# Optimization experiments

Measured on AMD Instinct MI355X. Metric: run time of the kernel, lower is better.

The kernel has to match this reference:

```python
import jax, jax.numpy as jnp
import numpy as np
import math

B, T, C, TF, N, DK = 4, 2048, 768, 128, 8, 96  # DK = max(C//8,16)

def _tau_init(Tw):
    alpha = 0.1 ** (1.0 / max(Tw - 1, 1))
    tau = -math.log(max(alpha, 1e-10))
    return math.log(math.exp(tau) - 1 + 1e-10)

def setup_inputs() -> dict:
    key = jax.random.key(0)
    ks = jax.random.split(key, 13)
    w = lambda k, shp: jax.random.normal(k, shp, jnp.float32) * 0.02
    return {
        'x': jax.random.normal(ks[0], (B, T, C), jnp.float32),
        'tau_gate': jnp.float32(_tau_init(max(T // 2, 4))),
        'tau_fast': jnp.float32(_tau_init(TF)),
        'tau_slow': jnp.float32(_tau_init(T)),
        'Wp': w(ks[1], (C, C)), 'bp': jnp.zeros((C,), jnp.float32),
        'Wxf': w(ks[2], (C, C)), 'bxf': jnp.full((C,), -0.5, jnp.float32),
        'Wxs': w(ks[3], (C, C)), 'bxs': jnp.full((C,), 0.5, jnp.float32),
        'Wcf': w(ks[4], (C, C)), 'Wcs': w(ks[5], (C, C)),
        'Wq': w(ks[6], (DK, C)), 'Wk': w(ks[7], (DK, C)),
        'Wfast': w(ks[8], (C, C)), 'bfast': jnp.zeros((C,), jnp.float32),
        'Wslow': w(ks[9], (C, C)), 'bslow': jnp.zeros((C,), jnp.float32),
        'Wsoma': w(ks[10], (C, C)), 'bsoma': jnp.zeros((C,), jnp.float32),
        'Wanc': w(ks[11], (C, C)), 'banc': jnp.zeros((C,), jnp.float32),
        'anchor_scales': jnp.linspace(1.5, -1.5, N).astype(jnp.float32),
        'blend_raw': jnp.zeros((1,), jnp.float32),
        'ln_g': jnp.ones((C,), jnp.float32), 'ln_b': jnp.zeros((C,), jnp.float32),
    }

def _lin(x, W, b=None):
    # torch Linear: y = x @ W.T + b, W is (out, in)
    y = jnp.einsum('btc,oc->bto', x, W)
    return y if b is None else y + b

def _ema(b, tau_raw):
    # exact h_t = alpha*h_{t-1} + b_t, h_{-1}=0 (same math as full causal conv with kernel alpha^j)
    alpha = jnp.exp(-jax.nn.softplus(tau_raw))
    def step(h, bt):
        h = alpha * h + bt
        return h, h
    _, hs = jax.lax.scan(step, jnp.zeros_like(b[:, 0, :]), jnp.swapaxes(b, 0, 1))
    return jnp.swapaxes(hs, 0, 1)  # (B,T,C)

def _forward(x, tau_gate, tau_fast, tau_slow, Wp, bp, Wxf, bxf, Wxs, bxs, Wcf, Wcs,
             Wq, Wk, Wfast, bfast, Wslow, bslow, Wsoma, bsoma, Wanc, banc,
             anchor_scales, blend_raw, ln_g, ln_b):
    x_proj = jnp.tanh(_lin(x, Wp, bp))
    ctx_gate = _ema(x, tau_gate)
    wg_f = jax.nn.sigmoid(_lin(x, Wxf, bxf) + _lin(ctx_gate, Wcf))
    wg_s = jax.nn.sigmoid(_lin(x, Wxs, bxs) + _lin(ctx_gate, Wcs))
    ctx_fast = _ema(x_proj * wg_f, tau_fast)
    ctx_slow = _ema(x_proj * wg_s, tau_slow)
    # F1 content gate: causal max-score sigmoid
    q = _lin(x, Wq)
    k = _lin(x, Wk)
    sc = jnp.einsum('btd,bsd->bts', q, k) * (DK ** -0.5)
    tril = jnp.tril(jnp.ones((T, T), bool))
    sc = jnp.where(tril[None], sc, -jnp.inf)
    cg = jax.nn.sigmoid(jnp.max(sc, axis=-1, keepdims=True))  # (B,T,1)
    ctx_fast = ctx_fast * cg
    ctx_slow = ctx_slow * cg
    # F5 anchors (static positions)
    pos = np.array([min(i * (T // N), T - 1) for i in range(N)])
    a = jnp.tanh(jnp.einsum('bnc,oc->bno', x[:, pos, :], Wanc) + banc)  # (B,N,C)
    delta = jnp.einsum('n,bnc->bc', jax.nn.sigmoid(anchor_scales), a)
    ctx_fast = ctx_fast + delta[:, None, :]
    ctx_slow = ctx_slow + delta[:, None, :]
    # F6 blend of fast/slow gates (torch.lerp)
    bl = jax.nn.sigmoid(blend_raw)  # (1,)
    gf = jax.nn.sigmoid(_lin(ctx_fast, Wfast, bfast))
    gs = jax.nn.sigmoid(_lin(ctx_slow, Wslow, bslow))
    gate = gf + bl * (gs - gf)
    soma = jnp.tanh(_lin(x, Wsoma, bsoma))
    y = soma * gate
    mu = jnp.mean(y, -1, keepdims=True)
    var = jnp.var(y, -1, keepdims=True)
    return (y - mu) / jnp.sqrt(var + 1e-5) * ln_g + ln_b  # dropout p=0 -> identity

def reference(x, tau_gate, tau_fast, tau_slow, Wp, bp, Wxf, bxf, Wxs, bxs, Wcf, Wcs,
              Wq, Wk, Wfast, bfast, Wslow, bslow, Wsoma, bsoma, Wanc, banc,
              anchor_scales, blend_raw, ln_g, ln_b):
    return _forward(x, tau_gate, tau_fast, tau_slow, Wp, bp, Wxf, bxf, Wxs, bxs, Wcf, Wcs,
                    Wq, Wk, Wfast, bfast, Wslow, bslow, Wsoma, bsoma, Wanc, banc,
                    anchor_scales, blend_raw, ln_g, ln_b)
```

## Files before the change

kernel.cpp:

```cpp
#include <hip/hip_runtime.h>
#include <math.h>

#define B_ 4
#define T_ 2048
#define C_ 768
#define DK_ 96
#define NA_ 8
#define M_ (B_*T_)
#define K2_ (2*C_)
#define NCH_ 256
#define CK_ 8

typedef __attribute__((ext_vector_type(8))) _Float16 half8;
typedef __attribute__((ext_vector_type(4))) _Float16 half4;
typedef __attribute__((ext_vector_type(4))) float floatx4;

#define AS1 __attribute__((address_space(1)))
#define AS3 __attribute__((address_space(3)))

__device__ __forceinline__ float sigm(float x){
  return __builtin_amdgcn_rcpf(1.f + __expf(-x));
}
__device__ __forceinline__ float ftanh(float x){
  return 1.f - 2.f*__builtin_amdgcn_rcpf(1.f + __expf(2.f*x));
}
__device__ __forceinline__ unsigned enc_max(float f){
  unsigned i = __float_as_uint(f);
  return (i & 0x80000000u) ? ~i : (i | 0x80000000u);
}
__device__ __forceinline__ float dec_max(unsigned u){
  unsigned i = (u & 0x80000000u) ? (u & 0x7FFFFFFFu) : ~u;
  return __uint_as_float(i);
}
__device__ __forceinline__ void gld16(const _Float16* g, _Float16* l){
  __builtin_amdgcn_global_load_lds((const AS1 unsigned int*)g, (AS3 unsigned int*)l, 16, 0, 0);
}

__device__ __forceinline__ void scan2l(const float* __restrict__ S, float* __restrict__ H,
                                       int b, int cg0, float aCK, float A16,
                                       float* __restrict__ carry ){
  int tid = threadIdx.x;
  int cl = tid & 15, g = tid >> 4;
  int c = cg0 + cl;
  float sv[16];
  float cv = 0.f;
  #pragma unroll
  for (int j = 0; j < 16; ++j){
    sv[j] = S[(size_t)(b*NCH_ + g*16 + j)*C_ + c];
    cv = aCK*cv + sv[j];
  }
  carry[cl*17 + g] = cv;
  __syncthreads();
  float h = 0.f;
  for (int gp = 0; gp < g; ++gp) h = A16*h + carry[cl*17 + gp];
  #pragma unroll
  for (int j = 0; j < 16; ++j){
    H[(size_t)(b*NCH_ + g*16 + j)*C_ + c] = h;
    h = aCK*h + sv[j];
  }
}

__global__ __launch_bounds__(192) void k_castx(
    const float* __restrict__ x, const float* __restrict__ tau,
    _Float16* __restrict__ xh, float* __restrict__ Sg){
  float al = expf(-log1pf(expf(tau[0])));
  int blk = blockIdx.x, b = blk >> 8, ch = blk & (NCH_-1);
  int t0 = b*T_ + ch*CK_;
  int c4 = threadIdx.x;
  float s0=0.f,s1=0.f,s2=0.f,s3=0.f;
  #pragma unroll
  for (int t = 0; t < CK_; ++t){
    float4 v = *(const float4*)(x + (size_t)(t0+t)*C_ + c4*4);
    half4 h = { (_Float16)v.x,(_Float16)v.y,(_Float16)v.z,(_Float16)v.w };
    *(half4*)(xh + (size_t)(t0+t)*C_ + c4*4) = h;
    s0 = al*s0 + v.x; s1 = al*s1 + v.y; s2 = al*s2 + v.z; s3 = al*s3 + v.w;
  }
  float4 sv = { s0,s1,s2,s3 };
  *(float4*)(Sg + (size_t)blk*C_ + c4*4) = sv;
}

#define NB0 4608
#define NB1 4896
#define NB2 4920
#define NB3 5112
__global__ __launch_bounds__(256) void k_prep(
    const float* __restrict__ x,
    const float* __restrict__ Wp, const float* __restrict__ Wfast,
    const float* __restrict__ Wslow, const float* __restrict__ Wsoma,
    const float* __restrict__ Wxf, const float* __restrict__ Wxs,
    const float* __restrict__ Wcf, const float* __restrict__ Wcs,
    const float* __restrict__ Wq, const float* __restrict__ Wk,
    const float* __restrict__ Wanc, const float* __restrict__ banc,
    const float* __restrict__ ascl, const float* __restrict__ tau_gate,
    const float* __restrict__ Sg,
    _Float16* __restrict__ wall, _Float16* __restrict__ wqk,
    unsigned* __restrict__ cgE, float* __restrict__ Hg, float* __restrict__ dlt)
{
  __shared__ float xs[NA_*C_];
  __shared__ float part[NA_*128];
  __shared__ float carry[16*17];
  int blk = blockIdx.x, tid = threadIdx.x;
  if (blk < NB0){
    int i = blk*256 + tid;
    const int per = (C_*C_)/4;
    int s = i / per, j = i - s*per;
    const float* src = s==0?Wp : s==1?Wfast : s==2?Wslow : s==3?Wsoma
                     : s==4?Wxf : s==5?Wxs : s==6?Wcf : Wcs;
    float4 v = ((const float4*)src)[j];
    half4 h = { (_Float16)v.x, (_Float16)v.y, (_Float16)v.z, (_Float16)v.w };
    ((half4*)wall)[(size_t)s*per + j] = h;
  } else if (blk < NB1){
    int sub = blk - NB0;
    if (sub >= 256){ cgE[(sub-256)*256 + tid] = 0u; return; }
    const float* src = (sub < 96) ? Wq + (size_t)sub*C_
                     : (sub < 192 ? Wk + (size_t)(sub-96)*C_ : nullptr);
    #pragma unroll
    for (int k = 0; k < 3; ++k){
      int c = tid + k*256;
      wqk[(size_t)sub*C_ + c] = src ? (_Float16)src[c] : (_Float16)0.f;
    }
  } else if (blk < NB2){
    int ab = blk - NB1;
    int ct = ab % 6, b = ab / 6;
    for (int i = tid; i < NA_*C_; i += 256){
      int n = i / C_, c = i - n*C_;
      xs[i] = x[(size_t)(b*T_ + n*(T_/NA_))*C_ + c];
    }
    __syncthreads();
    int col = ct*128 + (tid & 127), kh = tid >> 7;
    float acc[NA_] = {0,0,0,0,0,0,0,0};
    const float* wrow = Wanc + (size_t)col*C_ + kh*384;
    const float* xk = xs + kh*384;
    for (int k = 0; k < 384; ++k){
      float wv = wrow[k];
      #pragma unroll
      for (int n = 0; n < NA_; ++n) acc[n] += xk[n*C_ + k]*wv;
    }
    if (kh){
      #pragma unroll
      for (int n = 0; n < NA_; ++n) part[n*128 + (tid & 127)] = acc[n];
    }
    __syncthreads();
    if (!kh){
      float d = 0.f;
      float bv = banc[col];
      #pragma unroll
      for (int n = 0; n < NA_; ++n){
        float a = ftanh(acc[n] + part[n*128 + (tid & 127)] + bv);
        d += sigm(ascl[n]) * a;
      }
      dlt[(size_t)b*C_ + col] = d;
    }
  } else {
    int sub = blk - NB2;
    int b = sub / 48, cg0 = (sub - b*48)*16;
    float sp = log1pf(expf(tau_gate[0]));
    scan2l(Sg, Hg, b, cg0, expf(-8.f*sp), expf(-128.f*sp), carry);
  }
}

__global__ __launch_bounds__(256) void k_p2_fs(const float* __restrict__ Sf, const float* __restrict__ Ss,
                                               float* __restrict__ Hf, float* __restrict__ Hs,
                                               const float* __restrict__ tf, const float* __restrict__ ts){
  __shared__ float carry[16*17];
  int blk = blockIdx.x;
  int which = blk / (B_*48);
  int rem = blk - which*(B_*48);
  int b = rem / 48, cg0 = (rem - b*48)*16;
  float sp = log1pf(expf(which ? ts[0] : tf[0]));
  scan2l(which ? Ss : Sf, which ? Hs : Hf, b, cg0, expf(-8.f*sp), expf(-128.f*sp), carry);
}

__global__ __launch_bounds__(192) void k_gate_p3(
    const _Float16* __restrict__ xh, const float* __restrict__ H,
    const float* __restrict__ tau, _Float16* __restrict__ gate){
  float al = expf(-log1pf(expf(tau[0])));
  int blk = blockIdx.x, b = blk >> 8, ch = blk & (NCH_-1);
  int c4 = threadIdx.x;
  float4 h0 = *(const float4*)(H + (size_t)blk*C_ + c4*4);
  float g0=h0.x, g1=h0.y, g2=h0.z, g3=h0.w;
  int t0 = b*T_ + ch*CK_;
  #pragma unroll
  for (int t = 0; t < CK_; ++t){
    half4 v = *(const half4*)(xh + (size_t)(t0+t)*C_ + c4*4);
    g0 = al*g0 + (float)v[0]; g1 = al*g1 + (float)v[1];
    g2 = al*g2 + (float)v[2]; g3 = al*g3 + (float)v[3];
    half4 o = { (_Float16)g0,(_Float16)g1,(_Float16)g2,(_Float16)g3 };
    *(half4*)(gate + (size_t)(t0+t)*C_ + c4*4) = o;
  }
}

__global__ __launch_bounds__(192) void k_fs_p3(
    const _Float16* __restrict__ xph, _Float16* __restrict__ wgfs,
    const float* __restrict__ Hf, const float* __restrict__ Hs,
    const float* __restrict__ tf, const float* __restrict__ ts,
    const unsigned* __restrict__ cgE, const float* __restrict__ dlt){
  float af = expf(-log1pf(expf(tf[0])));
  float as = expf(-log1pf(expf(ts[0])));
  int blk = blockIdx.x, b = blk >> 8, ch = blk & (NCH_-1);
  int c4 = threadIdx.x;
  int t0 = b*T_ + ch*CK_;
  float4 hf4 = *(const float4*)(Hf + (size_t)blk*C_ + c4*4);
  float4 hs4 = *(const float4*)(Hs + (size_t)blk*C_ + c4*4);
  float4 d4  = *(const float4*)(dlt + (size_t)b*C_ + c4*4);
  float f0=hf4.x, f1=hf4.y, f2=hf4.z, f3=hf4.w;
  float e0=hs4.x, e1=hs4.y, e2=hs4.z, e3=hs4.w;
  float cgr[CK_];
  #pragma unroll
  for (int t = 0; t < CK_; ++t) cgr[t] = sigm(dec_max(cgE[t0+t]));
  #pragma unroll
  for (int t = 0; t < CK_; ++t){
    size_t rp = (size_t)(t0+t);
    half4 p  = *(const half4*)(xph  + rp*C_  + c4*4);
    half4 wf = *(const half4*)(wgfs + rp*K2_ + c4*4);
    half4 ws = *(const half4*)(wgfs + rp*K2_ + C_ + c4*4);
    f0 = af*f0 + (float)p[0]*(float)wf[0]; e0 = as*e0 + (float)p[0]*(float)ws[0];
    f1 = af*f1 + (float)p[1]*(float)wf[1]; e1 = as*e1 + (float)p[1]*(float)ws[1];
    f2 = af*f2 + (float)p[2]*(float)wf[2]; e2 = as*e2 + (float)p[2]*(float)ws[2];
    f3 = af*f3 + (float)p[3]*(float)wf[3]; e3 = as*e3 + (float)p[3]*(float)ws[3];
    float cg = cgr[t];
    half4 of = { (_Float16)(f0*cg + d4.x), (_Float16)(f1*cg + d4.y),
                 (_Float16)(f2*cg + d4.z), (_Float16)(f3*cg + d4.w) };
    half4 os = { (_Float16)(e0*cg + d4.x), (_Float16)(e1*cg + d4.y),
                 (_Float16)(e2*cg + d4.z), (_Float16)(e3*cg + d4.w) };
    *(half4*)(wgfs + rp*K2_ + c4*4) = of;
    *(half4*)(wgfs + rp*K2_ + C_ + c4*4) = os;
  }
}

__device__ __forceinline__ void stage_tile(const _Float16* __restrict__ src, int stride,
                                           int r0, int k0, _Float16* lds){
  int tid = threadIdx.x;
  int wave = tid >> 6, lane = tid & 63;
  #pragma unroll
  for (int it = 0; it < 4; ++it){
    int cb = it*256 + wave*64;
    int ck = cb + lane;
    int row = ck >> 3;
    int kp = (ck & 7) ^ (row & 7);
    gld16(src + (size_t)(r0+row)*stride + k0 + kp*8, lds + (size_t)cb*8);
  }
}

__device__ __forceinline__ void mfma_pass(const _Float16* As, const _Float16* Ws, floatx4 acc[4][4]){
  int tid = threadIdx.x;
  int wave = tid >> 6, lane = tid & 63;
  int wr = wave >> 1, wc = wave & 1;
  int lr = lane & 15, lq = lane >> 4;
  #pragma unroll
  for (int ks = 0; ks < 2; ++ks){
    half8 fa[4], fb[4];
    int off = (((ks*4 + lq) ^ (lr & 7)) << 3);
    #pragma unroll
    for (int i = 0; i < 4; ++i){
      fa[i] = *(const half8*)(As + (wr*64 + i*16 + lr)*64 + off);
      fb[i] = *(const half8*)(Ws + (wc*64 + i*16 + lr)*64 + off);
    }
    #pragma unroll
    for (int i = 0; i < 4; ++i)
      #pragma unroll
      for (int j = 0; j < 4; ++j)
        acc[i][j] = __builtin_amdgcn_mfma_f32_16x16x32_f16(fa[i], fb[j], acc[i][j], 0, 0, 0);
  }
}

__device__ __forceinline__ void store_tile_f16(floatx4 acc[4][4], _Float16* __restrict__ out, int ldo,
                                               const float* bias, const float* bias2,
                                               int m0, int n0, int act){
  int tid = threadIdx.x;
  int wave = tid >> 6, lane = tid & 63;
  int wr = wave >> 1, wc = wave & 1;
  int lr = lane & 15, lq = lane >> 4;
  #pragma unroll
  for (int i = 0; i < 4; ++i){
    #pragma unroll
    for (int j = 0; j < 4; ++j){
      int col = n0 + wc*64 + j*16 + lr;
      float bv = 0.f;
      if (bias) bv = (bias2 && col >= C_) ? bias2[col - C_] : bias[col];
      #pragma unroll
      for (int r = 0; r < 4; ++r){
        int rowm = m0 + wr*64 + i*16 + lq*4 + r;
        float z = acc[i][j][r] + bv;
        if (act == 1) z = ftanh(z);
        else if (act == 2) z = sigm(z);
        out[(size_t)rowm*ldo + col] = (_Float16)z;
      }
    }
  }
}

__global__ __launch_bounds__(256,4) void k_gemm_s3(
    const _Float16* __restrict__ xh, const _Float16* __restrict__ gate,
    const _Float16* __restrict__ wall, const _Float16* __restrict__ wqk,
    const float* __restrict__ bp, const float* __restrict__ bxf, const float* __restrict__ bxs,
    _Float16* __restrict__ xph, _Float16* __restrict__ wgfs, _Float16* __restrict__ qk)
{
  __shared__ _Float16 As[128*64];
  __shared__ _Float16 Ws[128*64];
  const size_t per = (size_t)C_*C_;
  floatx4 acc[4][4] = {};
  int m0 = blockIdx.x * 128;
  int ny = blockIdx.y;
  if (ny < 6){
    for (int k0 = 0; k0 < C_; k0 += 64){
      stage_tile(xh, C_, m0, k0, As);
      stage_tile(wall, C_, ny*128, k0, Ws);
      asm volatile("s_waitcnt vmcnt(0)" ::: "memory");
      __syncthreads();
      mfma_pass(As, Ws, acc);
      __syncthreads();
    }
    store_tile_f16(acc, xph, C_, bp, nullptr, m0, ny*128, 1);
  } else if (ny < 18){
    int n0 = (ny-6)*128;
    for (int k0 = 0; k0 < C_; k0 += 64){
      stage_tile(xh, C_, m0, k0, As);
      stage_tile(wall + 4*per, C_, n0, k0, Ws);
      asm volatile("s_waitcnt vmcnt(0)" ::: "memory");
      __syncthreads();
      mfma_pass(As, Ws, acc);
      __syncthreads();
    }
    for (int k0 = 0; k0 < C_; k0 += 64){
      stage_tile(gate, C_, m0, k0, As);
      stage_tile(wall + 6*per, C_, n0, k0, Ws);
      asm volatile("s_waitcnt vmcnt(0)" ::: "memory");
      __syncthreads();
      mfma_pass(As, Ws, acc);
      __syncthreads();
    }
    store_tile_f16(acc, wgfs, K2_, bxf, bxs, m0, n0, 2);
  } else {
    int n0 = (ny-18)*128;
    for (int k0 = 0; k0 < C_; k0 += 64){
      stage_tile(xh, C_, m0, k0, As);
      stage_tile(wqk, C_, n0, k0, Ws);
      asm volatile("s_waitcnt vmcnt(0)" ::: "memory");
      __syncthreads();
      mfma_pass(As, Ws, acc);
      __syncthreads();
    }
    store_tile_f16(acc, qk, 256, nullptr, nullptr, m0, n0, 0);
  }
}

__global__ __launch_bounds__(256,4) void k_gemm_s7(
    const _Float16* __restrict__ cfs, const _Float16* __restrict__ xh,
    const _Float16* __restrict__ wall,
    const float* __restrict__ bf, const float* __restrict__ bs, const float* __restrict__ bso,
    _Float16* __restrict__ gfb, _Float16* __restrict__ gsb, _Float16* __restrict__ somab)
{
  __shared__ _Float16 As[128*64];
  __shared__ _Float16 Bs[128*64];
  const size_t per = (size_t)C_*C_;
  floatx4 acc[4][4] = {};
  int m0 = blockIdx.x * 128;
  int s = blockIdx.y / 6, nt = (blockIdx.y % 6) * 128;
  const _Float16* Asrc = (s == 0) ? cfs : (s == 1 ? cfs + C_ : xh);
  int lda = (s == 2) ? C_ : K2_;
  const _Float16* Bsrc = wall + (size_t)(s+1)*per;
  for (int k0 = 0; k0 < C_; k0 += 64){
    stage_tile(Asrc, lda, m0, k0, As);
    stage_tile(Bsrc, C_, nt, k0, Bs);
    asm volatile("s_waitcnt vmcnt(0)" ::: "memory");
    __syncthreads();
    mfma_pass(As, Bs, acc);
    __syncthreads();
  }
  if (s == 2)      store_tile_f16(acc, somab, C_, bso, nullptr, m0, nt, 1);
  else if (s == 1) store_tile_f16(acc, gsb,  C_, bs,  nullptr, m0, nt, 2);
  else             store_tile_f16(acc, gfb,  C_, bf,  nullptr, m0, nt, 2);
}

#define SLDK 104
__global__ __launch_bounds__(256,3) void k_score_fs(
    const _Float16* __restrict__ qk, unsigned* __restrict__ cgE,
    const _Float16* __restrict__ xp, const _Float16* __restrict__ wgfs,
    const float* __restrict__ tf, const float* __restrict__ ts,
    float* __restrict__ Sf, float* __restrict__ Ss)
{
  __shared__ _Float16 Qs[128*SLDK];
  __shared__ _Float16 Ks[128*SLDK];
  __shared__ float sred[256];
  int idx = blockIdx.x;
  int tid = threadIdx.x;
  if (idx >= 544){
    if (tid >= 192) return;
    int f = idx - 544;
    float af = expf(-log1pf(expf(tf[0])));
    float as = expf(-log1pf(expf(ts[0])));
    int b = f >> 8, ch = f & (NCH_-1);
    int t0 = b*T_ + ch*CK_;
    float f0=0,f1=0,f2=0,f3=0, s0=0,s1=0,s2=0,s3=0;
    #pragma unroll
    for (int t = 0; t < CK_; ++t){
      half4 p = *(const half4*)(xp + (size_t)(t0+t)*C_ + tid*4);
      half4 wf = *(const half4*)(wgfs + (size_t)(t0+t)*K2_ + tid*4);
      half4 ws = *(const half4*)(wgfs + (size_t)(t0+t)*K2_ + C_ + tid*4);
      f0 = af*f0 + (float)p[0]*(float)wf[0]; s0 = as*s0 + (float)p[0]*(float)ws[0];
      f1 = af*f1 + (float)p[1]*(float)wf[1]; s1 = as*s1 + (float)p[1]*(float)ws[1];
      f2 = af*f2 + (float)p[2]*(float)wf[2]; s2 = as*s2 + (float)p[2]*(float)ws[2];
      f3 = af*f3 + (float)p[3]*(float)wf[3]; s3 = as*s3 + (float)p[3]*(float)ws[3];
    }
    float4 fv = { f0,f1,f2,f3 }, sv = { s0,s1,s2,s3 };
    *(float4*)(Sf + (size_t)f*C_ + tid*4) = fv;
    *(float4*)(Ss + (size_t)f*C_ + tid*4) = sv;
    return;
  }
  int b = idx / 136;
  int p = idx - b*136;
  int ti = (int)((sqrtf(8.f*p + 1.f) - 1.f)*0.5f);
  while ((ti+1)*(ti+2)/2 <= p) ++ti;
  while (ti*(ti+1)/2 > p) --ti;
  int sj = p - ti*(ti+1)/2;

  const _Float16* qg = qk + (size_t)(b*T_ + ti*128)*256;
  const _Float16* kg = qk + (size_t)(b*T_ + sj*128)*256 + 96;
  #pragma unroll
  for (int r = 0; r < 6; ++r){
    int ci = tid + r*256;
    int row = ci / 12, kp = ci % 12;
    *(uint4*)(&Qs[row*SLDK + kp*8]) = *(const uint4*)(qg + (size_t)row*256 + kp*8);
    *(uint4*)(&Ks[row*SLDK + kp*8]) = *(const uint4*)(kg + (size_t)row*256 + kp*8);
  }
  __syncthreads();

  int wave = tid >> 6, lane = tid & 63;
  int wr = wave >> 1, wc = wave & 1;
  int lr = lane & 15, lq = lane >> 4;
  floatx4 acc[4][4] = {};
  #pragma unroll
  for (int ks = 0; ks < 3; ++ks){
    half8 fa[4], fb[4];
    #pragma unroll
    for (int i = 0; i < 4; ++i){
      fa[i] = *(const half8*)(&Qs[(wr*64 + i*16 + lr)*SLDK + ks*32 + lq*8]);
      fb[i] = *(const half8*)(&Ks[(wc*64 + i*16 + lr)*SLDK + ks*32 + lq*8]);
    }
    #pragma unroll
    for (int i = 0; i < 4; ++i)
      #pragma unroll
      for (int j = 0; j < 4; ++j)
        acc[i][j] = __builtin_amdgcn_mfma_f32_16x16x32_f16(fa[i], fb[j], acc[i][j], 0, 0, 0);
  }
  const float scale = 0.10206207f;
  #pragma unroll
  for (int i = 0; i < 4; ++i){
    #pragma unroll
    for (int r = 0; r < 4; ++r){
      int row64 = i*16 + lq*4 + r;
      int tg = ti*128 + wr*64 + row64;
      float v = -3.0e38f;
      #pragma unroll
      for (int j = 0; j < 4; ++j){
        int sg = sj*128 + wc*64 + j*16 + lr;
        if (sg <= tg) v = fmaxf(v, acc[i][j][r]*scale);
      }
      #pragma unroll
      for (int off = 1; off < 16; off <<= 1) v = fmaxf(v, __shfl_xor(v, off, 16));
      if (lr == 0) sred[wr*128 + wc*64 + row64] = v;
    }
  }
  __syncthreads();
  if (wc == 0 && lane < 64){
    int row64 = lane;
    float v = fmaxf(sred[wr*128 + row64], sred[wr*128 + 64 + row64]);
    int tg = ti*128 + wr*64 + row64;
    atomicMax(&cgE[(size_t)b*T_ + tg], enc_max(v));
  }
}

__global__ __launch_bounds__(256) void k_ln(const _Float16* __restrict__ gfb,
                                            const _Float16* __restrict__ gsb,
                                            const _Float16* __restrict__ somab,
                                            const float* __restrict__ blendr,
                                            const float* __restrict__ g, const float* __restrict__ be,
                                            float* __restrict__ out){
  int wave = threadIdx.x >> 6, lane = threadIdx.x & 63;
  int row = blockIdx.x*4 + wave;
  float bl = sigm(blendr[0]);
  size_t rb = (size_t)row*C_;
  float v[12];
  float s = 0.f, ss = 0.f;
  #pragma unroll
  for (int w2 = 0; w2 < 3; ++w2){
    size_t o = rb + w2*256 + lane*4;
    half4 gf4 = *(const half4*)(gfb + o);
    half4 gs4 = *(const half4*)(gsb + o);
    half4 so4 = *(const half4*)(somab + o);
    #pragma unroll
    for (int i = 0; i < 4; ++i){
      float gf = (float)gf4[i], gs = (float)gs4[i], so = (float)so4[i];
      float y = so * (gf + bl*(gs - gf));
      v[w2*4 + i] = y; s += y; ss += y*y;
    }
  }
  #pragma unroll
  for (int off = 1; off < 64; off <<= 1){ s += __shfl_xor(s, off); ss += __shfl_xor(ss, off); }
  float mu  = s * (1.f/C_);
  float var = ss * (1.f/C_) - mu*mu;
  float inv = rsqrtf(var + 1e-5f);
  #pragma unroll
  for (int w2 = 0; w2 < 3; ++w2){
    int c0 = w2*256 + lane*4;
    float4 o4;
    o4.x = (v[w2*4+0]-mu)*inv*g[c0+0] + be[c0+0];
    o4.y = (v[w2*4+1]-mu)*inv*g[c0+1] + be[c0+1];
    o4.z = (v[w2*4+2]-mu)*inv*g[c0+2] + be[c0+2];
    o4.w = (v[w2*4+3]-mu)*inv*g[c0+3] + be[c0+3];
    *(float4*)(out + rb + c0) = o4;
  }
}

extern "C" void kernel_launch(void* const* d_in, const int* in_sizes, int n_in,
                              void* d_out, int out_size, void* d_ws, size_t ws_size,
                              hipStream_t stream){
  (void)in_sizes; (void)n_in; (void)out_size;
  const float* x        = (const float*)d_in[0];
  const float* tau_gate = (const float*)d_in[1];
  const float* tau_fast = (const float*)d_in[2];
  const float* tau_slow = (const float*)d_in[3];
  const float* Wp   = (const float*)d_in[4];  const float* bp    = (const float*)d_in[5];
  const float* Wxf  = (const float*)d_in[6];  const float* bxf   = (const float*)d_in[7];
  const float* Wxs  = (const float*)d_in[8];  const float* bxs   = (const float*)d_in[9];
  const float* Wcf  = (const float*)d_in[10]; const float* Wcs   = (const float*)d_in[11];
  const float* Wq   = (const float*)d_in[12]; const float* Wk    = (const float*)d_in[13];
  const float* Wfast= (const float*)d_in[14]; const float* bfast = (const float*)d_in[15];
  const float* Wslow= (const float*)d_in[16]; const float* bslow = (const float*)d_in[17];
  const float* Wsoma= (const float*)d_in[18]; const float* bsoma = (const float*)d_in[19];
  const float* Wanc = (const float*)d_in[20]; const float* banc  = (const float*)d_in[21];
  const float* ascl = (const float*)d_in[22]; const float* blendr= (const float*)d_in[23];
  const float* lng  = (const float*)d_in[24]; const float* lnb   = (const float*)d_in[25];
  float* out = (float*)d_out;

  char* w = (char*)d_ws;
  auto alloc = [&](size_t bytes)->void*{
    void* p = (void*)w; w += (bytes + 255) & ~(size_t)255; return p;
  };
  _Float16* xh    = (_Float16*)alloc((size_t)M_*C_*2);
  _Float16* wall  = (_Float16*)alloc((size_t)8*C_*C_*2);
  _Float16* wqk   = (_Float16*)alloc((size_t)256*C_*2);
  _Float16* xph   = (_Float16*)alloc((size_t)M_*C_*2);
  _Float16* wgfs  = (_Float16*)alloc((size_t)M_*K2_*2);
  _Float16* qk    = (_Float16*)alloc((size_t)M_*256*2);
  _Float16* gfb   = (_Float16*)alloc((size_t)M_*C_*2);
  _Float16* gsb   = (_Float16*)alloc((size_t)M_*C_*2);
  _Float16* somab = (_Float16*)alloc((size_t)M_*C_*2);
  unsigned* cgE   = (unsigned*)alloc((size_t)M_*4);
  float* Sg = (float*)alloc((size_t)B_*NCH_*C_*4);
  float* Hg = (float*)alloc((size_t)B_*NCH_*C_*4);
  float* Ss = (float*)alloc((size_t)B_*NCH_*C_*4);
  float* Hs = (float*)alloc((size_t)B_*NCH_*C_*4);
  float* dlt = (float*)alloc((size_t)B_*C_*4);
  _Float16* gate = gfb;
  float* Sf = Sg;
  float* Hf = Hg;
  if ((size_t)(w - (char*)d_ws) > ws_size) return;

  k_castx<<<B_*NCH_, 192, 0, stream>>>(x, tau_gate, xh, Sg);
  k_prep<<<NB3, 256, 0, stream>>>(x, Wp, Wfast, Wslow, Wsoma, Wxf, Wxs, Wcf, Wcs, Wq, Wk,
                                  Wanc, banc, ascl, tau_gate, Sg, wall, wqk, cgE, Hg, dlt);
  k_gate_p3<<<B_*NCH_, 192, 0, stream>>>(xh, Hg, tau_gate, gate);
  k_gemm_s3<<<dim3(M_/128, 20), 256, 0, stream>>>(xh, gate, wall, wqk,
                                                  bp, bxf, bxs, xph, wgfs, qk);
  k_score_fs<<<544 + B_*NCH_, 256, 0, stream>>>(qk, cgE, xph, wgfs, tau_fast, tau_slow, Sf, Ss);
  k_p2_fs<<<2*B_*48, 256, 0, stream>>>(Sf, Ss, Hf, Hs, tau_fast, tau_slow);
  k_fs_p3<<<B_*NCH_, 192, 0, stream>>>(xph, wgfs, Hf, Hs, tau_fast, tau_slow, cgE, dlt);
  k_gemm_s7<<<dim3(M_/128, 18), 256, 0, stream>>>(wgfs, xh, wall,
                                                  bfast, bslow, bsoma, gfb, gsb, somab);
  k_ln<<<M_/4, 256, 0, stream>>>(gfb, gsb, somab, blendr, lng, lnb, out);
}
```

Before: 328.6 us.

## Fuse three-phase chunked EMA scans into single kernels with global atomic barriers

Merges the cast/chunk-sum, carry scan, and gate-apply phases of the gate EMA into one kernel, and merges the fast/slow carry scan with its apply phase into another. In-kernel grid-wide barriers use sharded atomic counters with sleep-polling in place of separate kernel launches, and the x half-precision values are kept in registers rather than reloaded. This removes launch gaps and one reread of xh. The design assumes all 1024 blocks are co-resident (launch_bounds 256,4 on the available CUs); if they are not, it can deadlock. It also adds a memset and spin-wait overhead.

```diff
diff --git a/kernel.cpp b/kernel.cpp
--- a/kernel.cpp
+++ b/kernel.cpp
@@ -36,6 +36,28 @@
   __builtin_amdgcn_global_load_lds((const AS1 unsigned int*)g, (AS3 unsigned int*)l, 16, 0, 0);
 }
 
+#define SH_W 64
+__device__ __forceinline__ void pub(unsigned* base, int shard){
+  __syncthreads();
+  if (threadIdx.x == 0){
+    __threadfence();
+    atomicAdd(base + (size_t)shard*SH_W, 1u);
+  }
+}
+__device__ __forceinline__ void waitcnt(unsigned* base, int nsh, unsigned target){
+  if (threadIdx.x == 0){
+    for (;;){
+      unsigned s = 0;
+      for (int i = 0; i < nsh; ++i)
+        s += __hip_atomic_load(base + (size_t)i*SH_W, __ATOMIC_RELAXED, __HIP_MEMORY_SCOPE_AGENT);
+      if (s >= target) break;
+      __builtin_amdgcn_s_sleep(32);
+    }
+  }
+  __syncthreads();
+  __threadfence();
+}
+
 __device__ __forceinline__ void scan2l(const float* __restrict__ S, float* __restrict__ H,
                                        int b, int cg0, float aCK, float A16,
                                        float* __restrict__ carry ){
@@ -60,29 +82,57 @@
   }
 }
 
-__global__ __launch_bounds__(192) void k_castx(
-    const float* __restrict__ x, const float* __restrict__ tau,
-    _Float16* __restrict__ xh, float* __restrict__ Sg){
-  float al = expf(-log1pf(expf(tau[0])));
-  int blk = blockIdx.x, b = blk >> 8, ch = blk & (NCH_-1);
+__global__ __launch_bounds__(256,4) void k_castgate(
+    const float* __restrict__ x, const float* __restrict__ tau_gate,
+    _Float16* __restrict__ xh, float* __restrict__ Sg,
+    float* __restrict__ Hg, _Float16* __restrict__ gate,
+    unsigned* __restrict__ sync)
+{
+  __shared__ float carry[16*17];
+  int blk = blockIdx.x, tid = threadIdx.x;
+  int b = blk >> 8, ch = blk & (NCH_-1);
   int t0 = b*T_ + ch*CK_;
-  int c4 = threadIdx.x;
-  float s0=0.f,s1=0.f,s2=0.f,s3=0.f;
-  #pragma unroll
-  for (int t = 0; t < CK_; ++t){
-    float4 v = *(const float4*)(x + (size_t)(t0+t)*C_ + c4*4);
-    half4 h = { (_Float16)v.x,(_Float16)v.y,(_Float16)v.z,(_Float16)v.w };
-    *(half4*)(xh + (size_t)(t0+t)*C_ + c4*4) = h;
-    s0 = al*s0 + v.x; s1 = al*s1 + v.y; s2 = al*s2 + v.z; s3 = al*s3 + v.w;
-  }
-  float4 sv = { s0,s1,s2,s3 };
-  *(float4*)(Sg + (size_t)blk*C_ + c4*4) = sv;
+  int c4 = tid;
+  float al = expf(-log1pf(expf(tau_gate[0])));
+  half4 v8[CK_];
+  if (tid < 192){
+    float s0=0.f,s1=0.f,s2=0.f,s3=0.f;
+    #pragma unroll
+    for (int t = 0; t < CK_; ++t){
+      float4 v = *(const float4*)(x + (size_t)(t0+t)*C_ + c4*4);
+      half4 h = { (_Float16)v.x,(_Float16)v.y,(_Float16)v.z,(_Float16)v.w };
+      *(half4*)(xh + (size_t)(t0+t)*C_ + c4*4) = h;
+      v8[t] = h;
+      s0 = al*s0 + v.x; s1 = al*s1 + v.y; s2 = al*s2 + v.z; s3 = al*s3 + v.w;
+    }
+    float4 sv = { s0,s1,s2,s3 };
+    *(float4*)(Sg + (size_t)blk*C_ + c4*4) = sv;
+  }
+  pub(sync, blk & 31);
+  if (blk < 192){
+    waitcnt(sync, 32, 1024);
+    int sb = blk / 48, cg0 = (blk - sb*48)*16;
+    float sp = log1pf(expf(tau_gate[0]));
+    scan2l(Sg, Hg, sb, cg0, expf(-8.f*sp), expf(-128.f*sp), carry);
+    pub(sync + 32*SH_W, blk & 7);
+  }
+  waitcnt(sync + 32*SH_W, 8, 192);
+  if (tid < 192){
+    float4 h0 = *(const float4*)(Hg + (size_t)blk*C_ + c4*4);
+    float g0=h0.x, g1=h0.y, g2=h0.z, g3=h0.w;
+    #pragma unroll
+    for (int t = 0; t < CK_; ++t){
+      g0 = al*g0 + (float)v8[t][0]; g1 = al*g1 + (float)v8[t][1];
+      g2 = al*g2 + (float)v8[t][2]; g3 = al*g3 + (float)v8[t][3];
+      half4 o = { (_Float16)g0,(_Float16)g1,(_Float16)g2,(_Float16)g3 };
+      *(half4*)(gate + (size_t)(t0+t)*C_ + c4*4) = o;
+    }
+  }
 }
 
 #define NB0 4608
 #define NB1 4896
 #define NB2 4920
-#define NB3 5112
 __global__ __launch_bounds__(256) void k_prep(
     const float* __restrict__ x,
     const float* __restrict__ Wp, const float* __restrict__ Wfast,
@@ -91,14 +141,12 @@
     const float* __restrict__ Wcf, const float* __restrict__ Wcs,
     const float* __restrict__ Wq, const float* __restrict__ Wk,
     const float* __restrict__ Wanc, const float* __restrict__ banc,
-    const float* __restrict__ ascl, const float* __restrict__ tau_gate,
-    const float* __restrict__ Sg,
+    const float* __restrict__ ascl,
     _Float16* __restrict__ wall, _Float16* __restrict__ wqk,
-    unsigned* __restrict__ cgE, float* __restrict__ Hg, float* __restrict__ dlt)
+    unsigned* __restrict__ cgE, float* __restrict__ dlt)
 {
   __shared__ float xs[NA_*C_];
   __shared__ float part[NA_*128];
-  __shared__ float carry[16*17];
   int blk = blockIdx.x, tid = threadIdx.x;
   if (blk < NB0){
     int i = blk*256 + tid;
@@ -119,7 +167,7 @@
       int c = tid + k*256;
       wqk[(size_t)sub*C_ + c] = src ? (_Float16)src[c] : (_Float16)0.f;
     }
-  } else if (blk < NB2){
+  } else {
     int ab = blk - NB1;
     int ct = ab % 6, b = ab / 6;
     for (int i = tid; i < NA_*C_; i += 256){
@@ -151,80 +199,6 @@
       }
       dlt[(size_t)b*C_ + col] = d;
     }
-  } else {
-    int sub = blk - NB2;
-    int b = sub / 48, cg0 = (sub - b*48)*16;
-    float sp = log1pf(expf(tau_gate[0]));
-    scan2l(Sg, Hg, b, cg0, expf(-8.f*sp), expf(-128.f*sp), carry);
-  }
-}
-
-__global__ __launch_bounds__(256) void k_p2_fs(const float* __restrict__ Sf, const float* __restrict__ Ss,
-                                               float* __restrict__ Hf, float* __restrict__ Hs,
-                                               const float* __restrict__ tf, const float* __restrict__ ts){
-  __shared__ float carry[16*17];
-  int blk = blockIdx.x;
-  int which = blk / (B_*48);
-  int rem = blk - which*(B_*48);
-  int b = rem / 48, cg0 = (rem - b*48)*16;
-  float sp = log1pf(expf(which ? ts[0] : tf[0]));
-  scan2l(which ? Ss : Sf, which ? Hs : Hf, b, cg0, expf(-8.f*sp), expf(-128.f*sp), carry);
-}
-
-__global__ __launch_bounds__(192) void k_gate_p3(
-    const _Float16* __restrict__ xh, const float* __restrict__ H,
-    const float* __restrict__ tau, _Float16* __restrict__ gate){
-  float al = expf(-log1pf(expf(tau[0])));
-  int blk = blockIdx.x, b = blk >> 8, ch = blk & (NCH_-1);
-  int c4 = threadIdx.x;
-  float4 h0 = *(const float4*)(H + (size_t)blk*C_ + c4*4);
-  float g0=h0.x, g1=h0.y, g2=h0.z, g3=h0.w;
-  int t0 = b*T_ + ch*CK_;
-  #pragma unroll
-  for (int t = 0; t < CK_; ++t){
-    half4 v = *(const half4*)(xh + (size_t)(t0+t)*C_ + c4*4);
-    g0 = al*g0 + (float)v[0]; g1 = al*g1 + (float)v[1];
-    g2 = al*g2 + (float)v[2]; g3 = al*g3 + (float)v[3];
-    half4 o = { (_Float16)g0,(_Float16)g1,(_Float16)g2,(_Float16)g3 };
-    *(half4*)(gate + (size_t)(t0+t)*C_ + c4*4) = o;
-  }
-}
-
-__global__ __launch_bounds__(192) void k_fs_p3(
-    const _Float16* __restrict__ xph, _Float16* __restrict__ wgfs,
-    const float* __restrict__ Hf, const float* __restrict__ Hs,
-    const float* __restrict__ tf, const float* __restrict__ ts,
-    const unsigned* __restrict__ cgE, const float* __restrict__ dlt){
-  float af = expf(-log1pf(expf(tf[0])));
-  float as = expf(-log1pf(expf(ts[0])));
-  int blk = blockIdx.x, b = blk >> 8, ch = blk & (NCH_-1);
-  int c4 = threadIdx.x;
-  int t0 = b*T_ + ch*CK_;
-  float4 hf4 = *(const float4*)(Hf + (size_t)blk*C_ + c4*4);
-  float4 hs4 = *(const float4*)(Hs + (size_t)blk*C_ + c4*4);
-  float4 d4  = *(const float4*)(dlt + (size_t)b*C_ + c4*4);
-  float f0=hf4.x, f1=hf4.y, f2=hf4.z, f3=hf4.w;
-  float e0=hs4.x, e1=hs4.y, e2=hs4.z, e3=hs4.w;
-  float cgr[CK_];
-  #pragma unroll
-  for (int t = 0; t < CK_; ++t) cgr[t] = sigm(dec_max(cgE[t0+t]));
-  #pragma unroll
-  for (int t = 0; t < CK_; ++t){
-    size_t rp = (size_t)(t0+t);
-    half4 p  = *(const half4*)(xph  + rp*C_  + c4*4);
-    half4 wf = *(const half4*)(wgfs + rp*K2_ + c4*4);
-    half4 ws = *(const half4*)(wgfs + rp*K2_ + C_ + c4*4);
-    f0 = af*f0 + (float)p[0]*(float)wf[0]; e0 = as*e0 + (float)p[0]*(float)ws[0];
-    f1 = af*f1 + (float)p[1]*(float)wf[1]; e1 = as*e1 + (float)p[1]*(float)ws[1];
-    f2 = af*f2 + (float)p[2]*(float)wf[2]; e2 = as*e2 + (float)p[2]*(float)ws[2];
-    f3 = af*f3 + (float)p[3]*(float)wf[3]; e3 = as*e3 + (float)p[3]*(float)ws[3];
-    float cg = cgr[t];
-    half4 of = { (_Float16)(f0*cg + d4.x), (_Float16)(f1*cg + d4.y),
-                 (_Float16)(f2*cg + d4.z), (_Float16)(f3*cg + d4.w) };
-    half4 os = { (_Float16)(e0*cg + d4.x), (_Float16)(e1*cg + d4.y),
-                 (_Float16)(e2*cg + d4.z), (_Float16)(e3*cg + d4.w) };
-    *(half4*)(wgfs + rp*K2_ + c4*4) = of;
-    *(half4*)(wgfs + rp*K2_ + C_ + c4*4) = os;
   }
 }
 
@@ -471,6 +445,60 @@
   }
 }
 
+__global__ __launch_bounds__(256,4) void k_fsfused(
+    const _Float16* __restrict__ xp, _Float16* __restrict__ wgfs,
+    const float* __restrict__ Sf, const float* __restrict__ Ss,
+    float* __restrict__ Hf, float* __restrict__ Hs,
+    const float* __restrict__ tf, const float* __restrict__ ts,
+    const unsigned* __restrict__ cgE, const float* __restrict__ dlt,
+    unsigned* __restrict__ sync)
+{
+  __shared__ float carry[16*17];
+  int blk = blockIdx.x, tid = threadIdx.x;
+  float af = expf(-log1pf(expf(tf[0])));
+  float as = expf(-log1pf(expf(ts[0])));
+  if (blk < 384){
+    int which = blk / 192;
+    int rem = blk - which*192;
+    int sb = rem / 48, cg0 = (rem - sb*48)*16;
+    float sp = log1pf(expf(which ? ts[0] : tf[0]));
+    scan2l(which ? Ss : Sf, which ? Hs : Hf, sb, cg0, expf(-8.f*sp), expf(-128.f*sp), carry);
+    pub(sync + 40*SH_W, blk & 7);
+  }
+  waitcnt(sync + 40*SH_W, 8, 384);
+  if (tid < 192){
+    int b = blk >> 8, ch = blk & (NCH_-1);
+    int c4 = tid;
+    int t0 = b*T_ + ch*CK_;
+    float4 hf4 = *(const float4*)(Hf + (size_t)blk*C_ + c4*4);
+    float4 hs4 = *(const float4*)(Hs + (size_t)blk*C_ + c4*4);
+    float4 d4  = *(const float4*)(dlt + (size_t)b*C_ + c4*4);
+    float f0=hf4.x, f1=hf4.y, f2=hf4.z, f3=hf4.w;
+    float e0=hs4.x, e1=hs4.y, e2=hs4.z, e3=hs4.w;
+    float cgr[CK_];
+    #pragma unroll
+    for (int t = 0; t < CK_; ++t) cgr[t] = sigm(dec_max(cgE[t0+t]));
+    #pragma unroll
+    for (int t = 0; t < CK_; ++t){
+      size_t rp = (size_t)(t0+t);
+      half4 p  = *(const half4*)(xp   + rp*C_  + c4*4);
+      half4 wf = *(const half4*)(wgfs + rp*K2_ + c4*4);
+      half4 ws = *(const half4*)(wgfs + rp*K2_ + C_ + c4*4);
+      f0 = af*f0 + (float)p[0]*(float)wf[0]; e0 = as*e0 + (float)p[0]*(float)ws[0];
+      f1 = af*f1 + (float)p[1]*(float)wf[1]; e1 = as*e1 + (float)p[1]*(float)ws[1];
+      f2 = af*f2 + (float)p[2]*(float)wf[2]; e2 = as*e2 + (float)p[2]*(float)ws[2];
+      f3 = af*f3 + (float)p[3]*(float)wf[3]; e3 = as*e3 + (float)p[3]*(float)ws[3];
+      float cg = cgr[t];
+      half4 of = { (_Float16)(f0*cg + d4.x), (_Float16)(f1*cg + d4.y),
+                   (_Float16)(f2*cg + d4.z), (_Float16)(f3*cg + d4.w) };
+      half4 os = { (_Float16)(e0*cg + d4.x), (_Float16)(e1*cg + d4.y),
+                   (_Float16)(e2*cg + d4.z), (_Float16)(e3*cg + d4.w) };
+      *(half4*)(wgfs + rp*K2_ + c4*4) = of;
+      *(half4*)(wgfs + rp*K2_ + C_ + c4*4) = os;
+    }
+  }
+}
+
 __global__ __launch_bounds__(256) void k_ln(const _Float16* __restrict__ gfb,
                                             const _Float16* __restrict__ gsb,
                                             const _Float16* __restrict__ somab,
@@ -553,20 +581,21 @@
   float* Ss = (float*)alloc((size_t)B_*NCH_*C_*4);
   float* Hs = (float*)alloc((size_t)B_*NCH_*C_*4);
   float* dlt = (float*)alloc((size_t)B_*C_*4);
+  unsigned* sync = (unsigned*)alloc((size_t)48*SH_W*4);
   _Float16* gate = gfb;
   float* Sf = Sg;
   float* Hf = Hg;
   if ((size_t)(w - (char*)d_ws) > ws_size) return;
 
-  k_castx<<<B_*NCH_, 192, 0, stream>>>(x, tau_gate, xh, Sg);
-  k_prep<<<NB3, 256, 0, stream>>>(x, Wp, Wfast, Wslow, Wsoma, Wxf, Wxs, Wcf, Wcs, Wq, Wk,
-                                  Wanc, banc, ascl, tau_gate, Sg, wall, wqk, cgE, Hg, dlt);
-  k_gate_p3<<<B_*NCH_, 192, 0, stream>>>(xh, Hg, tau_gate, gate);
+  hipMemsetAsync(sync, 0, (size_t)48*SH_W*4, stream);
+  k_castgate<<<1024, 256, 0, stream>>>(x, tau_gate, xh, Sg, Hg, gate, sync);
+  k_prep<<<NB2, 256, 0, stream>>>(x, Wp, Wfast, Wslow, Wsoma, Wxf, Wxs, Wcf, Wcs, Wq, Wk,
+                                  Wanc, banc, ascl, wall, wqk, cgE, dlt);
   k_gemm_s3<<<dim3(M_/128, 20), 256, 0, stream>>>(xh, gate, wall, wqk,
                                                   bp, bxf, bxs, xph, wgfs, qk);
   k_score_fs<<<544 + B_*NCH_, 256, 0, stream>>>(qk, cgE, xph, wgfs, tau_fast, tau_slow, Sf, Ss);
-  k_p2_fs<<<2*B_*48, 256, 0, stream>>>(Sf, Ss, Hf, Hs, tau_fast, tau_slow);
-  k_fs_p3<<<B_*NCH_, 192, 0, stream>>>(xph, wgfs, Hf, Hs, tau_fast, tau_slow, cgE, dlt);
+  k_fsfused<<<1024, 256, 0, stream>>>(xph, wgfs, Sf, Ss, Hf, Hs, tau_fast, tau_slow,
+                                      cgE, dlt, sync);
   k_gemm_s7<<<dim3(M_/128, 18), 256, 0, stream>>>(wgfs, xh, wall,
                                                   bfast, bslow, bsoma, gfb, gsb, somab);
   k_ln<<<M_/4, 256, 0, stream>>>(gfb, gsb, somab, blendr, lng, lnb, out);
```

New measurement: 545.5 us. +66.0%, slower.
